# Kernel tuning notes

Hardware: AMD Instinct MI355X
Metric: run time of the kernel (lower is better)

Reference implementation:

```python
import jax, jax.numpy as jnp
import numpy as np

B, L, D, DIN, A, V, R = 1024, 100, 256, 704, 128, 32000, 129


def setup_inputs() -> dict:
    key = jax.random.key(0)
    ks = jax.random.split(key, 18)
    s = 0.05
    inp = {
        "x": jax.random.normal(ks[0], (B, DIN), jnp.float32),
        "h0": jax.random.normal(ks[1], (B, D), jnp.float32),
        "c0": jax.random.normal(ks[2], (B, D), jnp.float32),
        "src_enc": jax.random.normal(ks[3], (B, L, D), jnp.float32),
        "src_token_ids": jax.random.randint(ks[4], (B, L), 0, V),
        "W_ih": jax.random.normal(ks[5], (4 * D, DIN), jnp.float32) * s,
        "b_ih": jax.random.normal(ks[6], (4 * D,), jnp.float32) * s,
        "W_hh": jax.random.normal(ks[7], (4 * D, D), jnp.float32) * s,
        "b_hh": jax.random.normal(ks[8], (4 * D,), jnp.float32) * s,
        "W_attn": jax.random.normal(ks[9], (D, D), jnp.float32) * s,
        "W_att_vec": jax.random.normal(ks[10], (A * 2, 2 * D), jnp.float32) * s,
        "W_ptr": jax.random.normal(ks[11], (D, D), jnp.float32) * s,
        "rule_emb": jax.random.normal(ks[12], (R, 128), jnp.float32) * s,
        "W_rule_proj": jax.random.normal(ks[13], (D, 128), jnp.float32) * s,
        "prim_emb": jax.random.normal(ks[14], (V, 128), jnp.float32) * s,
        "W_prim_proj": jax.random.normal(ks[15], (D, 128), jnp.float32) * s,
        "w_gen": jax.random.normal(ks[16], (2, D), jnp.float32) * s,
        "b_gen": jax.random.normal(ks[17], (2,), jnp.float32) * s,
    }
    # W_att_vec maps concat(h, ctx) [2D] -> ATT (=256); keep shape (256, 512)
    inp["W_att_vec"] = inp["W_att_vec"][:256]
    return inp


def reference(x, h0, c0, src_enc, src_token_ids, W_ih, b_ih, W_hh, b_hh,
              W_attn, W_att_vec, W_ptr, rule_emb, W_rule_proj,
              prim_emb, W_prim_proj, w_gen, b_gen):
    # --- LSTMCell (torch gate order i, f, g, o) ---
    gates = x @ W_ih.T + b_ih + h0 @ W_hh.T + b_hh          # [B, 4D]
    i, f, g, o = jnp.split(gates, 4, axis=-1)
    i, f, o = jax.nn.sigmoid(i), jax.nn.sigmoid(f), jax.nn.sigmoid(o)
    c = f * c0 + i * jnp.tanh(g)
    h = o * jnp.tanh(c)                                      # [B, D]

    # --- dot-product attention over source encodings ---
    enc_proj = src_enc @ W_attn.T                            # [B, L, D]
    scores = jnp.einsum('bd,bld->bl', h, enc_proj)
    alpha = jax.nn.softmax(scores, axis=-1)
    ctx = jnp.einsum('bl,bld->bd', alpha, src_enc)
    att = jnp.tanh(jnp.concatenate([h, ctx], axis=-1) @ W_att_vec.T)  # [B, 256]

    # --- apply-rule (production) readout ---
    rule_proj = rule_emb @ W_rule_proj.T                     # [R, 256]
    log_p_rule = jax.nn.log_softmax(att @ rule_proj.T, axis=-1)  # [B, R]

    # --- primitive generation readout ---
    prim_proj = prim_emb @ W_prim_proj.T                     # [V, 256]
    p_gen_prim = jax.nn.softmax(att @ prim_proj.T, axis=-1)  # [B, V]

    # --- pointer network copy distribution over source positions ---
    ptr_scores = jnp.einsum('bld,bd->bl', src_enc @ W_ptr.T, att)
    copy_p = jax.nn.softmax(ptr_scores, axis=-1)             # [B, L]

    # --- gen vs copy gate (softmax over 2, per usage in parse()) ---
    gate = jax.nn.softmax(att @ w_gen.T + b_gen, axis=-1)    # [B, 2]

    # --- combined primitive distribution: gen + scattered copy mass ---
    p_prim = gate[:, :1] * p_gen_prim                        # [B, V]
    copy_mass = gate[:, 1:] * copy_p                         # [B, L]
    bidx = jnp.arange(p_prim.shape[0])[:, None]
    p_prim = p_prim.at[bidx, src_token_ids].add(copy_mass)
    return log_p_rule, p_prim, h, c, att
```

## Files before the change

### kernel.cpp

```cpp
#include <hip/hip_runtime.h>
#include <hip/hip_bf16.h>
#include <math.h>

#define NB   1024
#define LL   100
#define DD   256
#define DINN 704
#define VV   32000
#define RR   129
#define KAV  512
#define ROWU 129

typedef float f32x4 __attribute__((ext_vector_type(4)));
typedef float f32x2 __attribute__((ext_vector_type(2)));
typedef short s16x8 __attribute__((ext_vector_type(8)));
typedef unsigned short u16;
typedef unsigned int u32;

__device__ __forceinline__ float sigf(float x) { return 1.0f / (1.0f + __expf(-x)); }

__device__ __forceinline__ u16 f2bf(float f) {
    u32 u = __float_as_uint(f);
    u += 0x7fffu + ((u >> 16) & 1u);
    return (u16)(u >> 16);
}
__device__ __forceinline__ float bf2f(u16 s) {
    return __uint_as_float(((u32)s) << 16);
}

__global__ __launch_bounds__(256) void k_conv(
    const float* __restrict__ prim_emb, u16* __restrict__ prim_bf,
    const float* __restrict__ W_ih, u16* __restrict__ wih_bf,
    const float* __restrict__ W_hh, u16* __restrict__ whh_bf,
    const float* __restrict__ x, u16* __restrict__ x_bf,
    const float* __restrict__ h0, u16* __restrict__ h0_bf,
    const float* __restrict__ rule_emb, const float* __restrict__ W_rule_proj,
    float* __restrict__ rpT)
{
    __shared__ float re_s[128];
    const int bx = blockIdx.x, t = threadIdx.x;

    const float* src; u16* dst; int off;
    if (bx < 2000)      { src = prim_emb; dst = prim_bf; off = bx * 2048; }
    else if (bx < 2352) { src = W_ih;  dst = wih_bf; off = (bx - 2000) * 2048; }
    else if (bx < 2480) { src = W_hh;  dst = whh_bf; off = (bx - 2352) * 2048; }
    else if (bx < 2832) { src = x;     dst = x_bf;   off = (bx - 2480) * 2048; }
    else                { src = h0;    dst = h0_bf;  off = (bx - 2832) * 2048; }

    if (bx < RR && t < 128) re_s[t] = rule_emb[bx * 128 + t];

    int i = off + t * 8;
    f32x4 a = *reinterpret_cast<const f32x4*>(&src[i]);
    f32x4 b = *reinterpret_cast<const f32x4*>(&src[i + 4]);
    s16x8 r;
    r[0] = (short)f2bf(a[0]); r[1] = (short)f2bf(a[1]);
    r[2] = (short)f2bf(a[2]); r[3] = (short)f2bf(a[3]);
    r[4] = (short)f2bf(b[0]); r[5] = (short)f2bf(b[1]);
    r[6] = (short)f2bf(b[2]); r[7] = (short)f2bf(b[3]);
    *reinterpret_cast<s16x8*>(&dst[i]) = r;

    if (bx < RR) {
        __syncthreads();
        float acc = 0.f;
        const float* __restrict__ wr = &W_rule_proj[t * 128];
#pragma unroll 8
        for (int k = 0; k < 128; k += 4) {
            f32x4 w4 = *reinterpret_cast<const f32x4*>(&wr[k]);
            acc += w4[0] * re_s[k] + w4[1] * re_s[k + 1]
                 + w4[2] * re_s[k + 2] + w4[3] * re_s[k + 3];
        }
        rpT[t * 192 + bx] = acc;
    }
}

__global__ __launch_bounds__(256) void k_lstm(
    const u16* __restrict__ x_bf, const u16* __restrict__ h0_bf,
    const float* __restrict__ c0,
    const u16* __restrict__ wih_bf, const u16* __restrict__ whh_bf,
    const float* __restrict__ b_ih, const float* __restrict__ b_hh,
    float* __restrict__ out_h, float* __restrict__ out_c)
{
    const int t = threadIdx.x;
    const int lane = t & 63, w = t >> 6;
    const int lm = lane & 15, lq = lane >> 4;
    const int dg = blockIdx.x;
    const int row0 = blockIdx.y * 128 + w * 32;
    f32x4 acc[4][2] = {};

    for (int kt = 0; kt < 22; ++kt) {
        const int ko = kt * 32 + lq * 8;
        s16x8 bfr[4], afr[2];
#pragma unroll
        for (int mg = 0; mg < 4; ++mg)
            bfr[mg] = *reinterpret_cast<const s16x8*>(
                &wih_bf[(mg * 256 + dg * 16 + lm) * DINN + ko]);
#pragma unroll
        for (int ng = 0; ng < 2; ++ng)
            afr[ng] = *reinterpret_cast<const s16x8*>(
                &x_bf[(row0 + ng * 16 + lm) * DINN + ko]);
#pragma unroll
        for (int mg = 0; mg < 4; ++mg)
#pragma unroll
            for (int ng = 0; ng < 2; ++ng)
                acc[mg][ng] = __builtin_amdgcn_mfma_f32_16x16x32_bf16(
                    bfr[mg], afr[ng], acc[mg][ng], 0, 0, 0);
    }
    for (int kt = 0; kt < 8; ++kt) {
        const int ko = kt * 32 + lq * 8;
        s16x8 bfr[4], afr[2];
#pragma unroll
        for (int mg = 0; mg < 4; ++mg)
            bfr[mg] = *reinterpret_cast<const s16x8*>(
                &whh_bf[(mg * 256 + dg * 16 + lm) * DD + ko]);
#pragma unroll
        for (int ng = 0; ng < 2; ++ng)
            afr[ng] = *reinterpret_cast<const s16x8*>(
                &h0_bf[(row0 + ng * 16 + lm) * DD + ko]);
#pragma unroll
        for (int mg = 0; mg < 4; ++mg)
#pragma unroll
            for (int ng = 0; ng < 2; ++ng)
                acc[mg][ng] = __builtin_amdgcn_mfma_f32_16x16x32_bf16(
                    bfr[mg], afr[ng], acc[mg][ng], 0, 0, 0);
    }

    const int dc = dg * 16 + lq * 4;
    f32x4 bi[4];
#pragma unroll
    for (int mg = 0; mg < 4; ++mg) {
        f32x4 a4 = *reinterpret_cast<const f32x4*>(&b_ih[mg * 256 + dc]);
        f32x4 b4 = *reinterpret_cast<const f32x4*>(&b_hh[mg * 256 + dc]);
        bi[mg][0] = a4[0] + b4[0]; bi[mg][1] = a4[1] + b4[1];
        bi[mg][2] = a4[2] + b4[2]; bi[mg][3] = a4[3] + b4[3];
    }
#pragma unroll
    for (int ng = 0; ng < 2; ++ng) {
        const int row = row0 + ng * 16 + lm;
        f32x4 c4 = *reinterpret_cast<const f32x4*>(&c0[row * DD + dc]);
        f32x4 h4, cc4;
#pragma unroll
        for (int r = 0; r < 4; ++r) {
            float iv = acc[0][ng][r] + bi[0][r];
            float fv = acc[1][ng][r] + bi[1][r];
            float gv = acc[2][ng][r] + bi[2][r];
            float ov = acc[3][ng][r] + bi[3][r];
            float cc = sigf(fv) * c4[r] + sigf(iv) * tanhf(gv);
            cc4[r] = cc;
            h4[r] = sigf(ov) * tanhf(cc);
        }
        *reinterpret_cast<f32x4*>(&out_c[row * DD + dc]) = cc4;
        *reinterpret_cast<f32x4*>(&out_h[row * DD + dc]) = h4;
    }
}

__global__ __launch_bounds__(256) void k_hw(
    const float* __restrict__ h, const float* __restrict__ W_attn, float* __restrict__ hW)
{
    __shared__ __align__(16) float As[16][36];
    __shared__ __align__(16) float Bs[16][68];
    const int t = threadIdx.x;
    const int row0 = blockIdx.x * 32;
    const int col0 = blockIdx.y * 64;
    const int tr = t >> 4, tc = t & 15;
    float acc[2][4] = {};
    for (int kt = 0; kt < 16; ++kt) {
        __syncthreads();
#pragma unroll
        for (int p = 0; p < 2; ++p) {
            int e = t + p * 256;
            int r = e >> 4, kk = e & 15;
            As[kk][r] = h[(row0 + r) * DD + kt * 16 + kk];
        }
#pragma unroll
        for (int p = 0; p < 4; ++p) {
            int e = t + p * 256;
            int kk = e >> 6, c = e & 63;
            Bs[kk][c] = W_attn[(kt * 16 + kk) * DD + col0 + c];
        }
        __syncthreads();
#pragma unroll
        for (int kk = 0; kk < 16; ++kk) {
            float a0 = As[kk][tr * 2], a1 = As[kk][tr * 2 + 1];
            f32x4 b = *reinterpret_cast<const f32x4*>(&Bs[kk][tc * 4]);
#pragma unroll
            for (int i = 0; i < 4; ++i) {
                acc[0][i] = fmaf(a0, b[i], acc[0][i]);
                acc[1][i] = fmaf(a1, b[i], acc[1][i]);
            }
        }
    }
#pragma unroll
    for (int j = 0; j < 2; ++j) {
        f32x4 v;
#pragma unroll
        for (int i = 0; i < 4; ++i) v[i] = acc[j][i];
        *reinterpret_cast<f32x4*>(&hW[(row0 + tr * 2 + j) * DD + col0 + tc * 4]) = v;
    }
}

__global__ __launch_bounds__(256, 2) void k_attn2(
    const float* __restrict__ src_enc, const float* __restrict__ hW,
    float* __restrict__ ctx_out)
{
    __shared__ u32 enc_u[LL * ROWU];
    __shared__ __align__(16) float part[4][DD];
    __shared__ __align__(16) float hw_s[DD];
    __shared__ float sc_s[LL];
    __shared__ float al_s[LL];

    const int b = blockIdx.x, t = threadIdx.x;
    const int lane = t & 63, w = t >> 6;
    const float* __restrict__ enc = src_enc + (size_t)b * LL * DD;

    hw_s[t] = hW[b * DD + t];

#pragma unroll
    for (int p = 0; p < 25; ++p) {
        int q = p * 256 + t;
        int l = q >> 6, dq = q & 63;
        f32x4 ev = *reinterpret_cast<const f32x4*>(&enc[l * DD + dq * 4]);
        u32 w0 = (u32)f2bf(ev[0]) | ((u32)f2bf(ev[1]) << 16);
        u32 w1 = (u32)f2bf(ev[2]) | ((u32)f2bf(ev[3]) << 16);
        enc_u[l * ROWU + dq * 2]     = w0;
        enc_u[l * ROWU + dq * 2 + 1] = w1;
    }
    __syncthreads();

    {
        const int sl = ((w >> 1) << 6) + lane;
        float sp = 0.f;
        if (sl < LL) {
            const u32* __restrict__ rp = enc_u + sl * ROWU + ((w & 1) << 6);
            const float* __restrict__ hp = hw_s + ((w & 1) << 7);
#pragma unroll 32
            for (int k = 0; k < 64; ++k) {
                u32 v = rp[k];
                sp = fmaf(bf2f((u16)v),         hp[2 * k],     sp);
                sp = fmaf(bf2f((u16)(v >> 16)), hp[2 * k + 1], sp);
            }
        }
        part[w][lane] = sp;
    }
    __syncthreads();
    if (t < LL) sc_s[t] = part[(t >> 6) << 1][t & 63] + part[((t >> 6) << 1) + 1][t & 63];
    __syncthreads();

    if (w == 0) {
        float v0 = sc_s[lane];
        float v1 = (lane + 64 < LL) ? sc_s[lane + 64] : -1e30f;
        float m = fmaxf(v0, v1);
#pragma unroll
        for (int s = 1; s < 64; s <<= 1) m = fmaxf(m, __shfl_xor(m, s));
        float e0 = __expf(v0 - m);
        float e1 = (lane + 64 < LL) ? __expf(v1 - m) : 0.f;
        float ssum = e0 + e1;
#pragma unroll
        for (int s = 1; s < 64; s <<= 1) ssum += __shfl_xor(ssum, s);
        float inv = 1.f / ssum;
        al_s[lane] = e0 * inv;
        if (lane + 64 < LL) al_s[lane + 64] = e1 * inv;
    }
    __syncthreads();

    {
        const int l0 = w * 25;
        float c0 = 0.f, c1 = 0.f, c2 = 0.f, c3 = 0.f;
#pragma unroll
        for (int li = 0; li < 25; ++li) {
            int l = l0 + li;
            float a = al_s[l];
            u32 v0 = enc_u[l * ROWU + lane * 2];
            u32 v1 = enc_u[l * ROWU + lane * 2 + 1];
            c0 = fmaf(a, bf2f((u16)v0), c0);
            c1 = fmaf(a, bf2f((u16)(v0 >> 16)), c1);
            c2 = fmaf(a, bf2f((u16)v1), c2);
            c3 = fmaf(a, bf2f((u16)(v1 >> 16)), c3);
        }
        f32x4 p; p[0] = c0; p[1] = c1; p[2] = c2; p[3] = c3;
        *reinterpret_cast<f32x4*>(&part[w][lane * 4]) = p;
    }
    __syncthreads();
    ctx_out[b * DD + t] = (part[0][t] + part[1][t]) + (part[2][t] + part[3][t]);
}

__global__ __launch_bounds__(256) void k_att(
    const float* __restrict__ h, const float* __restrict__ ctx,
    const float* __restrict__ W_att_vec, float* __restrict__ att_out)
{
    __shared__ __align__(16) float As[16][36];
    __shared__ __align__(16) float Bs[16][68];
    const int t = threadIdx.x;
    const int row0 = blockIdx.x * 32;
    const int col0 = blockIdx.y * 64;
    const int tr = t >> 4, tc = t & 15;
    float acc[2][4] = {};
    for (int kt = 0; kt < 32; ++kt) {
        const float* __restrict__ Asrc = (kt < 16) ? h : ctx;
        int kb = (kt < 16) ? kt * 16 : (kt - 16) * 16;
        int kg = kt * 16;
        __syncthreads();
#pragma unroll
        for (int p = 0; p < 2; ++p) {
            int e = t + p * 256;
            int r = e >> 4, kk = e & 15;
            As[kk][r] = Asrc[(row0 + r) * DD + kb + kk];
        }
#pragma unroll
        for (int p = 0; p < 4; ++p) {
            int e = t + p * 256;
            int r = e >> 4, kk = e & 15;
            Bs[kk][r] = W_att_vec[(col0 + r) * KAV + kg + kk];
        }
        __syncthreads();
#pragma unroll
        for (int kk = 0; kk < 16; ++kk) {
            float a0 = As[kk][tr * 2], a1 = As[kk][tr * 2 + 1];
            f32x4 b = *reinterpret_cast<const f32x4*>(&Bs[kk][tc * 4]);
#pragma unroll
            for (int i = 0; i < 4; ++i) {
                acc[0][i] = fmaf(a0, b[i], acc[0][i]);
                acc[1][i] = fmaf(a1, b[i], acc[1][i]);
            }
        }
    }
#pragma unroll
    for (int j = 0; j < 2; ++j)
#pragma unroll
        for (int i = 0; i < 4; ++i)
            att_out[(row0 + tr * 2 + j) * DD + col0 + tc * 4 + i] = tanhf(acc[j][i]);
}

__global__ __launch_bounds__(256) void k_ptrproj(
    const float* __restrict__ att, const float* __restrict__ W_ptr,
    const float* __restrict__ W_prim_proj, const float* __restrict__ rpT,
    float* __restrict__ atw, u16* __restrict__ att_bf, float* __restrict__ rl)
{
    __shared__ __align__(16) float As[16][36];
    __shared__ __align__(16) float Bs[16][68];
    const int t = threadIdx.x;
    const int row0 = blockIdx.x * 32;
    const int col0 = blockIdx.y * 64;
    const int tr = t >> 4, tc = t & 15;
    float acc[2][4] = {};
    for (int kt = 0; kt < 16; ++kt) {
        __syncthreads();
#pragma unroll
        for (int p = 0; p < 2; ++p) {
            int e = t + p * 256;
            int r = e >> 4, kk = e & 15;
            As[kk][r] = att[(row0 + r) * DD + kt * 16 + kk];
        }
#pragma unroll
        for (int p = 0; p < 4; ++p) {
            int e = t + p * 256;
            int kk = e >> 6, c = e & 63;
            float bv;
            if (col0 < 256)      bv = W_ptr[(kt * 16 + kk) * DD + col0 + c];
            else if (col0 < 384) bv = W_prim_proj[(kt * 16 + kk) * 128 + (col0 - 256) + c];
            else {
                int rc = col0 - 384 + c;
                bv = (rc < RR) ? rpT[(kt * 16 + kk) * 192 + rc] : 0.f;
            }
            Bs[kk][c] = bv;
        }
        __syncthreads();
#pragma unroll
        for (int kk = 0; kk < 16; ++kk) {
            float a0 = As[kk][tr * 2], a1 = As[kk][tr * 2 + 1];
            f32x4 b = *reinterpret_cast<const f32x4*>(&Bs[kk][tc * 4]);
#pragma unroll
            for (int i = 0; i < 4; ++i) {
                acc[0][i] = fmaf(a0, b[i], acc[0][i]);
                acc[1][i] = fmaf(a1, b[i], acc[1][i]);
            }
        }
    }
    if (col0 < 256) {
#pragma unroll
        for (int j = 0; j < 2; ++j) {
            f32x4 v;
#pragma unroll
            for (int i = 0; i < 4; ++i) v[i] = acc[j][i];
            *reinterpret_cast<f32x4*>(&atw[(row0 + tr * 2 + j) * DD + col0 + tc * 4]) = v;
        }
    } else if (col0 < 384) {
#pragma unroll
        for (int j = 0; j < 2; ++j)
#pragma unroll
            for (int i = 0; i < 4; ++i)
                att_bf[(row0 + tr * 2 + j) * 128 + (col0 - 256) + tc * 4 + i] = f2bf(acc[j][i]);
    } else {
#pragma unroll
        for (int j = 0; j < 2; ++j)
#pragma unroll
            for (int i = 0; i < 4; ++i) {
                int rc = col0 - 384 + tc * 4 + i;
                if (rc < RR) rl[(row0 + tr * 2 + j) * 132 + rc] = acc[j][i];
            }
    }
}

__global__ __launch_bounds__(256) void k_fin(
    const float* __restrict__ rl, const float* __restrict__ att,
    const float* __restrict__ w_gen, const float* __restrict__ b_gen,
    float* __restrict__ log_p_rule, float* __restrict__ gate0_ws,
    float* __restrict__ gate1_ws)
{
    const int w = threadIdx.x >> 6, lane = threadIdx.x & 63;
    const int b = blockIdx.x * 4 + w;

    float v0 = rl[b * 132 + lane];
    float v1 = rl[b * 132 + 64 + lane];
    float v2 = (lane == 0) ? rl[b * 132 + 128] : -1e30f;
    float m = fmaxf(fmaxf(v0, v1), v2);
#pragma unroll
    for (int s = 1; s < 64; s <<= 1) m = fmaxf(m, __shfl_xor(m, s));
    float ssum = __expf(v0 - m) + __expf(v1 - m) + ((lane == 0) ? __expf(v2 - m) : 0.f);
#pragma unroll
    for (int s = 1; s < 64; s <<= 1) ssum += __shfl_xor(ssum, s);
    float ls = m + logf(ssum);
    log_p_rule[b * RR + lane] = v0 - ls;
    log_p_rule[b * RR + 64 + lane] = v1 - ls;
    if (lane == 0) log_p_rule[b * RR + 128] = v2 - ls;

    f32x4 a4 = *reinterpret_cast<const f32x4*>(&att[b * DD + lane * 4]);
    f32x4 g0 = *reinterpret_cast<const f32x4*>(&w_gen[lane * 4]);
    f32x4 g1 = *reinterpret_cast<const f32x4*>(&w_gen[DD + lane * 4]);
    float p0 = a4[0] * g0[0] + a4[1] * g0[1] + a4[2] * g0[2] + a4[3] * g0[3];
    float p1 = a4[0] * g1[0] + a4[1] * g1[1] + a4[2] * g1[2] + a4[3] * g1[3];
#pragma unroll
    for (int s = 1; s < 64; s <<= 1) { p0 += __shfl_xor(p0, s); p1 += __shfl_xor(p1, s); }
    if (lane == 0) {
        float ga = p0 + b_gen[0], gb = p1 + b_gen[1];
        float gm = fmaxf(ga, gb);
        float ea = __expf(ga - gm), eb = __expf(gb - gm);
        gate0_ws[b] = ea / (ea + eb);
        gate1_ws[b] = eb / (ea + eb);
    }
}

__global__ __launch_bounds__(256) void k_ptr2(
    const float* __restrict__ src_enc, const float* __restrict__ atw,
    const float* __restrict__ gate1_ws, float* __restrict__ copy_mass)
{
    __shared__ float sc_s[LL];
    const int b = blockIdx.x, t = threadIdx.x;
    const int lane = t & 63, w = t >> 6;
    const float* __restrict__ enc = src_enc + (size_t)b * LL * DD;
    f32x4 aw4 = *reinterpret_cast<const f32x4*>(&atw[b * DD + lane * 4]);

    for (int l = w; l < LL; l += 4) {
        f32x4 ev = *reinterpret_cast<const f32x4*>(&enc[l * DD + lane * 4]);
        float pr = aw4[0] * ev[0] + aw4[1] * ev[1] + aw4[2] * ev[2] + aw4[3] * ev[3];
#pragma unroll
        for (int m = 1; m < 64; m <<= 1) pr += __shfl_xor(pr, m);
        if (lane == 0) sc_s[l] = pr;
    }
    __syncthreads();
    if (w == 0) {
        float gate1 = gate1_ws[b];
        float v0 = sc_s[lane];
        float v1 = (lane + 64 < LL) ? sc_s[lane + 64] : -1e30f;
        float m = fmaxf(v0, v1);
#pragma unroll
        for (int s = 1; s < 64; s <<= 1) m = fmaxf(m, __shfl_xor(m, s));
        float ee0 = __expf(v0 - m);
        float ee1 = (lane + 64 < LL) ? __expf(v1 - m) : 0.f;
        float ssum = ee0 + ee1;
#pragma unroll
        for (int s = 1; s < 64; s <<= 1) ssum += __shfl_xor(ssum, s);
        float inv = 1.f / ssum;
        copy_mass[b * LL + lane] = gate1 * ee0 * inv;
        if (lane + 64 < LL) copy_mass[b * LL + lane + 64] = gate1 * ee1 * inv;
    }
}

template <int PASS>
__global__ __launch_bounds__(256) void k_prim(
    const u16* __restrict__ att_bf, const u16* __restrict__ prim_bf,
    const float* __restrict__ coef, float* __restrict__ stats, float* __restrict__ p_prim)
{
    const int t = threadIdx.x;
    const int lane = t & 63, w = t >> 6;
    const int lm = lane & 15, lq = lane >> 4;
    const int colbase = blockIdx.x * 128 + (w & 1) * 64;
    const int chunk = colbase >> 6;
    const int rowblk = blockIdx.y * 256;

    s16x8 pfr[4][4];
#pragma unroll
    for (int kg = 0; kg < 4; ++kg)
#pragma unroll
        for (int mg = 0; mg < 4; ++mg)
            pfr[kg][mg] = *reinterpret_cast<const s16x8*>(
                &prim_bf[(size_t)(colbase + mg * 16 + lm) * 128 + kg * 32 + lq * 8]);

    for (int it = 0; it < 2; ++it) {
        const int rowbase = rowblk + it * 128 + (w >> 1) * 64;
        f32x4 acc[4][4] = {};
#pragma unroll
        for (int kg = 0; kg < 4; ++kg) {
            s16x8 afr[4];
#pragma unroll
            for (int ng = 0; ng < 4; ++ng)
                afr[ng] = *reinterpret_cast<const s16x8*>(
                    &att_bf[(rowbase + ng * 16 + lm) * 128 + kg * 32 + lq * 8]);
#pragma unroll
            for (int mg = 0; mg < 4; ++mg)
#pragma unroll
                for (int ng = 0; ng < 4; ++ng)
                    acc[mg][ng] = __builtin_amdgcn_mfma_f32_16x16x32_bf16(
                        pfr[kg][mg], afr[ng], acc[mg][ng], 0, 0, 0);
        }
        if (PASS == 0) {
#pragma unroll
            for (int ng = 0; ng < 4; ++ng) {
                float se = 0.f;
#pragma unroll
                for (int mg = 0; mg < 4; ++mg)
                    se += __expf(acc[mg][ng][0]) + __expf(acc[mg][ng][1])
                        + __expf(acc[mg][ng][2]) + __expf(acc[mg][ng][3]);
                se += __shfl_xor(se, 16);
                se += __shfl_xor(se, 32);
                if (lq == 0)
                    stats[chunk * NB + rowbase + ng * 16 + lm] = se;
            }
        } else {
#pragma unroll
            for (int ng = 0; ng < 4; ++ng) {
                const int arow = rowbase + ng * 16 + lm;
                const float cf = coef[arow];
                float* __restrict__ dst = &p_prim[(size_t)arow * VV + colbase + lq * 4];
#pragma unroll
                for (int mg = 0; mg < 4; ++mg) {
                    f32x4 v;
                    v[0] = cf * __expf(acc[mg][ng][0]);
                    v[1] = cf * __expf(acc[mg][ng][1]);
                    v[2] = cf * __expf(acc[mg][ng][2]);
                    v[3] = cf * __expf(acc[mg][ng][3]);
                    *reinterpret_cast<f32x4*>(&dst[mg * 16]) = v;
                }
            }
        }
    }
}

__global__ __launch_bounds__(256) void k_combine(
    const float* __restrict__ stats, const float* __restrict__ gate0_ws,
    float* __restrict__ coef)
{
    const int row = blockIdx.x * 256 + threadIdx.x;
    float s0 = 0.f, s1 = 0.f, s2 = 0.f, s3 = 0.f;
    for (int c = 0; c < 500; c += 4) {
        s0 += stats[(c)     * NB + row];
        s1 += stats[(c + 1) * NB + row];
        s2 += stats[(c + 2) * NB + row];
        s3 += stats[(c + 3) * NB + row];
    }
    coef[row] = gate0_ws[row] / ((s0 + s1) + (s2 + s3));
}

__global__ __launch_bounds__(256) void k_scatter(
    const int* __restrict__ tok, const float* __restrict__ copy_mass, float* __restrict__ p_prim)
{
    int i = blockIdx.x * 256 + threadIdx.x;
    if (i >= NB * LL) return;
    int b = i / LL;
    atomicAdd(&p_prim[(size_t)b * VV + tok[i]], copy_mass[i]);
}

extern "C" void kernel_launch(void* const* d_in, const int* in_sizes, int n_in,
                              void* d_out, int out_size, void* d_ws, size_t ws_size,
                              hipStream_t stream)
{
    const float* x         = (const float*)d_in[0];
    const float* h0        = (const float*)d_in[1];
    const float* c0        = (const float*)d_in[2];
    const float* src_enc   = (const float*)d_in[3];
    const int*   tok       = (const int*)  d_in[4];
    const float* W_ih      = (const float*)d_in[5];
    const float* b_ih      = (const float*)d_in[6];
    const float* W_hh      = (const float*)d_in[7];
    const float* b_hh      = (const float*)d_in[8];
    const float* W_attn    = (const float*)d_in[9];
    const float* W_att_vec = (const float*)d_in[10];
    const float* W_ptr     = (const float*)d_in[11];
    const float* rule_emb  = (const float*)d_in[12];
    const float* W_rule_pr = (const float*)d_in[13];
    const float* prim_emb  = (const float*)d_in[14];
    const float* W_prim_pr = (const float*)d_in[15];
    const float* w_gen     = (const float*)d_in[16];
    const float* b_gen     = (const float*)d_in[17];

    float* out    = (float*)d_out;
    float* o_logp = out;
    float* o_pp   = out + 1024 * 129;
    float* o_h    = o_pp + (size_t)1024 * 32000;
    float* o_c    = o_h + 1024 * 256;
    float* o_att  = o_c + 1024 * 256;

    float* wsf      = (float*)d_ws;
    float* ws_rpT   = wsf;
    float* ws_rl    = ws_rpT   + 49152;
    float* ws_gate0 = ws_rl    + 135168;
    float* ws_gate1 = ws_gate0 + 1024;
    float* ws_cm    = ws_gate1 + 1024;
    float* ws_coef  = ws_cm    + 102400;
    float* ws_hw    = ws_coef  + 1024;
    float* ws_ctx   = ws_hw    + 262144;
    float* ws_atw   = ws_ctx   + 262144;
    float* ws_stats = ws_atw   + 262144;
    u16*   ub       = (u16*)(ws_stats + 512000);
    u16*   ws_attbf = ub;
    u16*   ws_primbf= ws_attbf + 131072;
    u16*   ws_xb    = ws_primbf + 4096000;
    u16*   ws_h0b   = ws_xb    + 720896;
    u16*   ws_wihb  = ws_h0b   + 262144;
    u16*   ws_whhb  = ws_wihb  + 720896;

    k_conv<<<dim3(2960), 256, 0, stream>>>(prim_emb, ws_primbf, W_ih, ws_wihb,
                                           W_hh, ws_whhb, x, ws_xb, h0, ws_h0b,
                                           rule_emb, W_rule_pr, ws_rpT);
    k_lstm<<<dim3(16, 8), 256, 0, stream>>>(ws_xb, ws_h0b, c0, ws_wihb, ws_whhb,
                                            b_ih, b_hh, o_h, o_c);
    k_hw<<<dim3(32, 4), 256, 0, stream>>>(o_h, W_attn, ws_hw);
    k_attn2<<<dim3(1024), 256, 0, stream>>>(src_enc, ws_hw, ws_ctx);
    k_att<<<dim3(32, 4), 256, 0, stream>>>(o_h, ws_ctx, W_att_vec, o_att);
    k_ptrproj<<<dim3(32, 9), 256, 0, stream>>>(o_att, W_ptr, W_prim_pr, ws_rpT,
                                               ws_atw, ws_attbf, ws_rl);
    k_fin<<<dim3(256), 256, 0, stream>>>(ws_rl, o_att, w_gen, b_gen,
                                         o_logp, ws_gate0, ws_gate1);
    k_ptr2<<<dim3(1024), 256, 0, stream>>>(src_enc, ws_atw, ws_gate1, ws_cm);
    k_prim<0><<<dim3(250, 4), 256, 0, stream>>>(ws_attbf, ws_primbf, nullptr, ws_stats, nullptr);
    k_combine<<<dim3(4), 256, 0, stream>>>(ws_stats, ws_gate0, ws_coef);
    k_prim<1><<<dim3(250, 4), 256, 0, stream>>>(ws_attbf, ws_primbf, ws_coef, nullptr, o_pp);
    k_scatter<<<dim3(400), 256, 0, stream>>>(tok, ws_cm, o_pp);
}
```

Measured before the change: 235.0 us.

## Move attention and projection GEMMs to bf16 MFMA with pre-transposed bf16 weights

```diff
diff --git a/kernel.cpp b/kernel.cpp
--- a/kernel.cpp
+++ b/kernel.cpp
@@ -12,7 +12,6 @@
 #define ROWU 129
 
 typedef float f32x4 __attribute__((ext_vector_type(4)));
-typedef float f32x2 __attribute__((ext_vector_type(2)));
 typedef short s16x8 __attribute__((ext_vector_type(8)));
 typedef unsigned short u16;
 typedef unsigned int u32;
@@ -34,18 +33,43 @@
     const float* __restrict__ W_hh, u16* __restrict__ whh_bf,
     const float* __restrict__ x, u16* __restrict__ x_bf,
     const float* __restrict__ h0, u16* __restrict__ h0_bf,
+    const float* __restrict__ W_att_vec, u16* __restrict__ wav_bf,
+    const float* __restrict__ W_attn, u16* __restrict__ wattnT,
+    const float* __restrict__ W_ptr, u16* __restrict__ wptrT,
+    const float* __restrict__ W_prim_proj, u16* __restrict__ wppT,
     const float* __restrict__ rule_emb, const float* __restrict__ W_rule_proj,
-    float* __restrict__ rpT)
+    u16* __restrict__ rp_bf)
 {
     __shared__ float re_s[128];
+    __shared__ __align__(16) float tile[64][65];
     const int bx = blockIdx.x, t = threadIdx.x;
 
+    if (bx >= 3024) {
+        const float* src; u16* dst; int S, D2, r0, c0;
+        if (bx < 3040) { int id = bx - 3024; src = W_attn; dst = wattnT;
+                         S = 256; D2 = 256; r0 = (id >> 2) * 64; c0 = (id & 3) * 64; }
+        else if (bx < 3056) { int id = bx - 3040; src = W_ptr; dst = wptrT;
+                         S = 256; D2 = 256; r0 = (id >> 2) * 64; c0 = (id & 3) * 64; }
+        else { int id = bx - 3056; src = W_prim_proj; dst = wppT;
+                         S = 128; D2 = 256; r0 = (id >> 1) * 64; c0 = (id & 1) * 64; }
+        const int rr = t >> 6, cc = t & 63;
+#pragma unroll
+        for (int p = 0; p < 16; ++p)
+            tile[rr + p * 4][cc] = src[(r0 + rr + p * 4) * S + c0 + cc];
+        __syncthreads();
+#pragma unroll
+        for (int p = 0; p < 16; ++p)
+            dst[(c0 + rr + p * 4) * D2 + r0 + cc] = f2bf(tile[cc][rr + p * 4]);
+        return;
+    }
+
     const float* src; u16* dst; int off;
-    if (bx < 2000)      { src = prim_emb; dst = prim_bf; off = bx * 2048; }
-    else if (bx < 2352) { src = W_ih;  dst = wih_bf; off = (bx - 2000) * 2048; }
-    else if (bx < 2480) { src = W_hh;  dst = whh_bf; off = (bx - 2352) * 2048; }
-    else if (bx < 2832) { src = x;     dst = x_bf;   off = (bx - 2480) * 2048; }
-    else                { src = h0;    dst = h0_bf;  off = (bx - 2832) * 2048; }
+    if (bx < 2000)      { src = prim_emb;  dst = prim_bf; off = bx * 2048; }
+    else if (bx < 2352) { src = W_ih;      dst = wih_bf;  off = (bx - 2000) * 2048; }
+    else if (bx < 2480) { src = W_hh;      dst = whh_bf;  off = (bx - 2352) * 2048; }
+    else if (bx < 2832) { src = x;         dst = x_bf;    off = (bx - 2480) * 2048; }
+    else if (bx < 2960) { src = h0;        dst = h0_bf;   off = (bx - 2832) * 2048; }
+    else                { src = W_att_vec; dst = wav_bf;  off = (bx - 2960) * 2048; }
 
     if (bx < RR && t < 128) re_s[t] = rule_emb[bx * 128 + t];
 
@@ -69,7 +93,7 @@
             acc += w4[0] * re_s[k] + w4[1] * re_s[k + 1]
                  + w4[2] * re_s[k + 2] + w4[3] * re_s[k + 3];
         }
-        rpT[t * 192 + bx] = acc;
+        rp_bf[bx * 256 + t] = f2bf(acc);
     }
 }
 
@@ -78,7 +102,8 @@
     const float* __restrict__ c0,
     const u16* __restrict__ wih_bf, const u16* __restrict__ whh_bf,
     const float* __restrict__ b_ih, const float* __restrict__ b_hh,
-    float* __restrict__ out_h, float* __restrict__ out_c)
+    float* __restrict__ out_h, float* __restrict__ out_c,
+    u16* __restrict__ h_bf)
 {
     const int t = threadIdx.x;
     const int lane = t & 63, w = t >> 6;
@@ -150,57 +175,55 @@
         }
         *reinterpret_cast<f32x4*>(&out_c[row * DD + dc]) = cc4;
         *reinterpret_cast<f32x4*>(&out_h[row * DD + dc]) = h4;
+        u32 w0 = (u32)f2bf(h4[0]) | ((u32)f2bf(h4[1]) << 16);
+        u32 w1 = (u32)f2bf(h4[2]) | ((u32)f2bf(h4[3]) << 16);
+        u32* hb = reinterpret_cast<u32*>(&h_bf[row * DD + dc]);
+        hb[0] = w0; hb[1] = w1;
     }
 }
 
 __global__ __launch_bounds__(256) void k_hw(
-    const float* __restrict__ h, const float* __restrict__ W_attn, float* __restrict__ hW)
-{
-    __shared__ __align__(16) float As[16][36];
-    __shared__ __align__(16) float Bs[16][68];
+    const u16* __restrict__ h_bf, const u16* __restrict__ wattnT,
+    float* __restrict__ hW)
+{
     const int t = threadIdx.x;
-    const int row0 = blockIdx.x * 32;
-    const int col0 = blockIdx.y * 64;
-    const int tr = t >> 4, tc = t & 15;
-    float acc[2][4] = {};
-    for (int kt = 0; kt < 16; ++kt) {
-        __syncthreads();
-#pragma unroll
-        for (int p = 0; p < 2; ++p) {
-            int e = t + p * 256;
-            int r = e >> 4, kk = e & 15;
-            As[kk][r] = h[(row0 + r) * DD + kt * 16 + kk];
-        }
-#pragma unroll
-        for (int p = 0; p < 4; ++p) {
-            int e = t + p * 256;
-            int kk = e >> 6, c = e & 63;
-            Bs[kk][c] = W_attn[(kt * 16 + kk) * DD + col0 + c];
-        }
-        __syncthreads();
-#pragma unroll
-        for (int kk = 0; kk < 16; ++kk) {
-            float a0 = As[kk][tr * 2], a1 = As[kk][tr * 2 + 1];
-            f32x4 b = *reinterpret_cast<const f32x4*>(&Bs[kk][tc * 4]);
-#pragma unroll
-            for (int i = 0; i < 4; ++i) {
-                acc[0][i] = fmaf(a0, b[i], acc[0][i]);
-                acc[1][i] = fmaf(a1, b[i], acc[1][i]);
-            }
-        }
-    }
-#pragma unroll
-    for (int j = 0; j < 2; ++j) {
-        f32x4 v;
-#pragma unroll
-        for (int i = 0; i < 4; ++i) v[i] = acc[j][i];
-        *reinterpret_cast<f32x4*>(&hW[(row0 + tr * 2 + j) * DD + col0 + tc * 4]) = v;
+    const int lane = t & 63, w = t >> 6;
+    const int lm = lane & 15, lq = lane >> 4;
+    const int colbase = blockIdx.x * 128 + (w & 1) * 64;
+    const int rowbase = blockIdx.y * 128 + (w >> 1) * 64;
+
+    f32x4 acc[4][4] = {};
+#pragma unroll
+    for (int kg = 0; kg < 8; ++kg) {
+        s16x8 pfr[4], afr[4];
+#pragma unroll
+        for (int mg = 0; mg < 4; ++mg)
+            pfr[mg] = *reinterpret_cast<const s16x8*>(
+                &wattnT[(colbase + mg * 16 + lm) * 256 + kg * 32 + lq * 8]);
+#pragma unroll
+        for (int ng = 0; ng < 4; ++ng)
+            afr[ng] = *reinterpret_cast<const s16x8*>(
+                &h_bf[(rowbase + ng * 16 + lm) * 256 + kg * 32 + lq * 8]);
+#pragma unroll
+        for (int mg = 0; mg < 4; ++mg)
+#pragma unroll
+            for (int ng = 0; ng < 4; ++ng)
+                acc[mg][ng] = __builtin_amdgcn_mfma_f32_16x16x32_bf16(
+                    pfr[mg], afr[ng], acc[mg][ng], 0, 0, 0);
+    }
+#pragma unroll
+    for (int ng = 0; ng < 4; ++ng) {
+        const int arow = rowbase + ng * 16 + lm;
+#pragma unroll
+        for (int mg = 0; mg < 4; ++mg)
+            *reinterpret_cast<f32x4*>(&hW[arow * DD + colbase + mg * 16 + lq * 4])
+                = acc[mg][ng];
     }
 }
 
 __global__ __launch_bounds__(256, 2) void k_attn2(
     const float* __restrict__ src_enc, const float* __restrict__ hW,
-    float* __restrict__ ctx_out)
+    u16* __restrict__ ctx_bf)
 {
     __shared__ u32 enc_u[LL * ROWU];
     __shared__ __align__(16) float part[4][DD];
@@ -280,123 +303,123 @@
         *reinterpret_cast<f32x4*>(&part[w][lane * 4]) = p;
     }
     __syncthreads();
-    ctx_out[b * DD + t] = (part[0][t] + part[1][t]) + (part[2][t] + part[3][t]);
+    ctx_bf[b * DD + t] = f2bf((part[0][t] + part[1][t]) + (part[2][t] + part[3][t]));
 }
 
 __global__ __launch_bounds__(256) void k_att(
-    const float* __restrict__ h, const float* __restrict__ ctx,
-    const float* __restrict__ W_att_vec, float* __restrict__ att_out)
-{
-    __shared__ __align__(16) float As[16][36];
-    __shared__ __align__(16) float Bs[16][68];
+    const u16* __restrict__ h_bf, const u16* __restrict__ ctx_bf,
+    const u16* __restrict__ wav_bf,
+    float* __restrict__ att_out, u16* __restrict__ att2_bf)
+{
     const int t = threadIdx.x;
-    const int row0 = blockIdx.x * 32;
-    const int col0 = blockIdx.y * 64;
-    const int tr = t >> 4, tc = t & 15;
-    float acc[2][4] = {};
-    for (int kt = 0; kt < 32; ++kt) {
-        const float* __restrict__ Asrc = (kt < 16) ? h : ctx;
-        int kb = (kt < 16) ? kt * 16 : (kt - 16) * 16;
-        int kg = kt * 16;
-        __syncthreads();
-#pragma unroll
-        for (int p = 0; p < 2; ++p) {
-            int e = t + p * 256;
-            int r = e >> 4, kk = e & 15;
-            As[kk][r] = Asrc[(row0 + r) * DD + kb + kk];
-        }
-#pragma unroll
-        for (int p = 0; p < 4; ++p) {
-            int e = t + p * 256;
-            int r = e >> 4, kk = e & 15;
-            Bs[kk][r] = W_att_vec[(col0 + r) * KAV + kg + kk];
-        }
-        __syncthreads();
-#pragma unroll
-        for (int kk = 0; kk < 16; ++kk) {
-            float a0 = As[kk][tr * 2], a1 = As[kk][tr * 2 + 1];
-            f32x4 b = *reinterpret_cast<const f32x4*>(&Bs[kk][tc * 4]);
-#pragma unroll
-            for (int i = 0; i < 4; ++i) {
-                acc[0][i] = fmaf(a0, b[i], acc[0][i]);
-                acc[1][i] = fmaf(a1, b[i], acc[1][i]);
+    const int lane = t & 63, w = t >> 6;
+    const int lm = lane & 15, lq = lane >> 4;
+    const int colbase = blockIdx.x * 128 + (w & 1) * 64;
+    const int rowbase = blockIdx.y * 128 + (w >> 1) * 64;
+
+    f32x4 acc[4][4] = {};
+#pragma unroll
+    for (int kg = 0; kg < 16; ++kg) {
+        const u16* __restrict__ asrc = (kg < 8) ? h_bf : ctx_bf;
+        const int ko = (kg & 7) * 32 + lq * 8;
+        s16x8 pfr[4], afr[4];
+#pragma unroll
+        for (int mg = 0; mg < 4; ++mg)
+            pfr[mg] = *reinterpret_cast<const s16x8*>(
+                &wav_bf[(colbase + mg * 16 + lm) * KAV + kg * 32 + lq * 8]);
+#pragma unroll
+        for (int ng = 0; ng < 4; ++ng)
+            afr[ng] = *reinterpret_cast<const s16x8*>(
+                &asrc[(rowbase + ng * 16 + lm) * 256 + ko]);
+#pragma unroll
+        for (int mg = 0; mg < 4; ++mg)
+#pragma unroll
+            for (int ng = 0; ng < 4; ++ng)
+                acc[mg][ng] = __builtin_amdgcn_mfma_f32_16x16x32_bf16(
+                    pfr[mg], afr[ng], acc[mg][ng], 0, 0, 0);
+    }
+#pragma unroll
+    for (int ng = 0; ng < 4; ++ng) {
+        const int arow = rowbase + ng * 16 + lm;
+#pragma unroll
+        for (int mg = 0; mg < 4; ++mg) {
+            const int col = colbase + mg * 16 + lq * 4;
+            f32x4 v;
+#pragma unroll
+            for (int r = 0; r < 4; ++r) v[r] = tanhf(acc[mg][ng][r]);
+            *reinterpret_cast<f32x4*>(&att_out[arow * DD + col]) = v;
+            u32 w0 = (u32)f2bf(v[0]) | ((u32)f2bf(v[1]) << 16);
+            u32 w1 = (u32)f2bf(v[2]) | ((u32)f2bf(v[3]) << 16);
+            u32* ab = reinterpret_cast<u32*>(&att2_bf[arow * DD + col]);
+            ab[0] = w0; ab[1] = w1;
+        }
+    }
+}
+
+__global__ __launch_bounds__(256) void k_ptrproj(
+    const u16* __restrict__ att2_bf, const u16* __restrict__ wptrT,
+    const u16* __restrict__ wppT, const u16* __restrict__ rp_bf,
+    float* __restrict__ atw, u16* __restrict__ att_bf, float* __restrict__ rl)
+{
+    const int t = threadIdx.x;
+    const int lane = t & 63, w = t >> 6;
+    const int lm = lane & 15, lq = lane >> 4;
+    const int gx = blockIdx.x;
+    const int colbase = gx * 128 + (w & 1) * 64;
+    const int rowbase = blockIdx.y * 128 + (w >> 1) * 64;
+
+    const u16* __restrict__ B;
+    int noff;
+    if (gx < 2)      { B = wptrT; noff = colbase; }
+    else if (gx < 3) { B = wppT;  noff = colbase - 256; }
+    else             { B = rp_bf; noff = colbase - 384; }
+
+    f32x4 acc[4][4] = {};
+#pragma unroll
+    for (int kg = 0; kg < 8; ++kg) {
+        s16x8 pfr[4], afr[4];
+#pragma unroll
+        for (int mg = 0; mg < 4; ++mg)
+            pfr[mg] = *reinterpret_cast<const s16x8*>(
+                &B[(noff + mg * 16 + lm) * 256 + kg * 32 + lq * 8]);
+#pragma unroll
+        for (int ng = 0; ng < 4; ++ng)
+            afr[ng] = *reinterpret_cast<const s16x8*>(
+                &att2_bf[(rowbase + ng * 16 + lm) * 256 + kg * 32 + lq * 8]);
+#pragma unroll
+        for (int mg = 0; mg < 4; ++mg)
+#pragma unroll
+            for (int ng = 0; ng < 4; ++ng)
+                acc[mg][ng] = __builtin_amdgcn_mfma_f32_16x16x32_bf16(
+                    pfr[mg], afr[ng], acc[mg][ng], 0, 0, 0);
+    }
+
+#pragma unroll
+    for (int ng = 0; ng < 4; ++ng) {
+        const int arow = rowbase + ng * 16 + lm;
+        if (gx < 2) {
+#pragma unroll
+            for (int mg = 0; mg < 4; ++mg)
+                *reinterpret_cast<f32x4*>(&atw[arow * DD + colbase + mg * 16 + lq * 4])
+                    = acc[mg][ng];
+        } else if (gx < 3) {
+#pragma unroll
+            for (int mg = 0; mg < 4; ++mg) {
+                const int col = noff + mg * 16 + lq * 4;
+                u32 w0 = (u32)f2bf(acc[mg][ng][0]) | ((u32)f2bf(acc[mg][ng][1]) << 16);
+                u32 w1 = (u32)f2bf(acc[mg][ng][2]) | ((u32)f2bf(acc[mg][ng][3]) << 16);
+                u32* ab = reinterpret_cast<u32*>(&att_bf[arow * 128 + col]);
+                ab[0] = w0; ab[1] = w1;
             }
-        }
-    }
-#pragma unroll
-    for (int j = 0; j < 2; ++j)
-#pragma unroll
-        for (int i = 0; i < 4; ++i)
-            att_out[(row0 + tr * 2 + j) * DD + col0 + tc * 4 + i] = tanhf(acc[j][i]);
-}
-
-__global__ __launch_bounds__(256) void k_ptrproj(
-    const float* __restrict__ att, const float* __restrict__ W_ptr,
-    const float* __restrict__ W_prim_proj, const float* __restrict__ rpT,
-    float* __restrict__ atw, u16* __restrict__ att_bf, float* __restrict__ rl)
-{
-    __shared__ __align__(16) float As[16][36];
-    __shared__ __align__(16) float Bs[16][68];
-    const int t = threadIdx.x;
-    const int row0 = blockIdx.x * 32;
-    const int col0 = blockIdx.y * 64;
-    const int tr = t >> 4, tc = t & 15;
-    float acc[2][4] = {};
-    for (int kt = 0; kt < 16; ++kt) {
-        __syncthreads();
-#pragma unroll
-        for (int p = 0; p < 2; ++p) {
-            int e = t + p * 256;
-            int r = e >> 4, kk = e & 15;
-            As[kk][r] = att[(row0 + r) * DD + kt * 16 + kk];
-        }
-#pragma unroll
-        for (int p = 0; p < 4; ++p) {
-            int e = t + p * 256;
-            int kk = e >> 6, c = e & 63;
-            float bv;
-            if (col0 < 256)      bv = W_ptr[(kt * 16 + kk) * DD + col0 + c];
-            else if (col0 < 384) bv = W_prim_proj[(kt * 16 + kk) * 128 + (col0 - 256) + c];
-            else {
-                int rc = col0 - 384 + c;
-                bv = (rc < RR) ? rpT[(kt * 16 + kk) * 192 + rc] : 0.f;
-            }
-            Bs[kk][c] = bv;
-        }
-        __syncthreads();
-#pragma unroll
-        for (int kk = 0; kk < 16; ++kk) {
-            float a0 = As[kk][tr * 2], a1 = As[kk][tr * 2 + 1];
-            f32x4 b = *reinterpret_cast<const f32x4*>(&Bs[kk][tc * 4]);
-#pragma unroll
-            for (int i = 0; i < 4; ++i) {
-                acc[0][i] = fmaf(a0, b[i], acc[0][i]);
-                acc[1][i] = fmaf(a1, b[i], acc[1][i]);
-            }
-        }
-    }
-    if (col0 < 256) {
-#pragma unroll
-        for (int j = 0; j < 2; ++j) {
-            f32x4 v;
-#pragma unroll
-            for (int i = 0; i < 4; ++i) v[i] = acc[j][i];
-            *reinterpret_cast<f32x4*>(&atw[(row0 + tr * 2 + j) * DD + col0 + tc * 4]) = v;
-        }
-    } else if (col0 < 384) {
-#pragma unroll
-        for (int j = 0; j < 2; ++j)
-#pragma unroll
-            for (int i = 0; i < 4; ++i)
-                att_bf[(row0 + tr * 2 + j) * 128 + (col0 - 256) + tc * 4 + i] = f2bf(acc[j][i]);
-    } else {
-#pragma unroll
-        for (int j = 0; j < 2; ++j)
-#pragma unroll
-            for (int i = 0; i < 4; ++i) {
-                int rc = col0 - 384 + tc * 4 + i;
-                if (rc < RR) rl[(row0 + tr * 2 + j) * 132 + rc] = acc[j][i];
-            }
+        } else {
+#pragma unroll
+            for (int mg = 0; mg < 4; ++mg)
+#pragma unroll
+                for (int r = 0; r < 4; ++r) {
+                    int rc = noff + mg * 16 + lq * 4 + r;
+                    if (rc < RR) rl[arow * 132 + rc] = acc[mg][ng][r];
+                }
+        }
     }
 }
 
@@ -561,7 +584,8 @@
 }
 
 __global__ __launch_bounds__(256) void k_scatter(
-    const int* __restrict__ tok, const float* __restrict__ copy_mass, float* __restrict__ p_prim)
+    const int* __restrict__ tok, const float* __restrict__ copy_mass,
+    float* __restrict__ p_prim)
 {
     int i = blockIdx.x * 256 + threadIdx.x;
     if (i >= NB * LL) return;
@@ -600,15 +624,13 @@
     float* o_att  = o_c + 1024 * 256;
 
     float* wsf      = (float*)d_ws;
-    float* ws_rpT   = wsf;
-    float* ws_rl    = ws_rpT   + 49152;
+    float* ws_rl    = wsf;
     float* ws_gate0 = ws_rl    + 135168;
     float* ws_gate1 = ws_gate0 + 1024;
     float* ws_cm    = ws_gate1 + 1024;
     float* ws_coef  = ws_cm    + 102400;
     float* ws_hw    = ws_coef  + 1024;
-    float* ws_ctx   = ws_hw    + 262144;
-    float* ws_atw   = ws_ctx   + 262144;
+    float* ws_atw   = ws_hw    + 262144;
     float* ws_stats = ws_atw   + 262144;
     u16*   ub       = (u16*)(ws_stats + 512000);
     u16*   ws_attbf = ub;
@@ -617,17 +639,27 @@
     u16*   ws_h0b   = ws_xb    + 720896;
     u16*   ws_wihb  = ws_h0b   + 262144;
     u16*   ws_whhb  = ws_wihb  + 720896;
-
-    k_conv<<<dim3(2960), 256, 0, stream>>>(prim_emb, ws_primbf, W_ih, ws_wihb,
+    u16*   ws_hbf   = ws_whhb  + 262144;
+    u16*   ws_ctxbf = ws_hbf   + 262144;
+    u16*   ws_att2  = ws_ctxbf + 262144;
+    u16*   ws_wavb  = ws_att2  + 262144;
+    u16*   ws_wattnT= ws_wavb  + 131072;
+    u16*   ws_wptrT = ws_wattnT+ 65536;
+    u16*   ws_wppT  = ws_wptrT + 65536;
+    u16*   ws_rpb   = ws_wppT  + 32768;
+
+    k_conv<<<dim3(3064), 256, 0, stream>>>(prim_emb, ws_primbf, W_ih, ws_wihb,
                                            W_hh, ws_whhb, x, ws_xb, h0, ws_h0b,
-                                           rule_emb, W_rule_pr, ws_rpT);
+                                           W_att_vec, ws_wavb, W_attn, ws_wattnT,
+                                           W_ptr, ws_wptrT, W_prim_pr, ws_wppT,
+                                           rule_emb, W_rule_pr, ws_rpb);
     k_lstm<<<dim3(16, 8), 256, 0, stream>>>(ws_xb, ws_h0b, c0, ws_wihb, ws_whhb,
-                                            b_ih, b_hh, o_h, o_c);
-    k_hw<<<dim3(32, 4), 256, 0, stream>>>(o_h, W_attn, ws_hw);
-    k_attn2<<<dim3(1024), 256, 0, stream>>>(src_enc, ws_hw, ws_ctx);
-    k_att<<<dim3(32, 4), 256, 0, stream>>>(o_h, ws_ctx, W_att_vec, o_att);
-    k_ptrproj<<<dim3(32, 9), 256, 0, stream>>>(o_att, W_ptr, W_prim_pr, ws_rpT,
-                                               ws_atw, ws_attbf, ws_rl);
+                                            b_ih, b_hh, o_h, o_c, ws_hbf);
+    k_hw<<<dim3(2, 8), 256, 0, stream>>>(ws_hbf, ws_wattnT, ws_hw);
+    k_attn2<<<dim3(1024), 256, 0, stream>>>(src_enc, ws_hw, ws_ctxbf);
+    k_att<<<dim3(2, 8), 256, 0, stream>>>(ws_hbf, ws_ctxbf, ws_wavb, o_att, ws_att2);
+    k_ptrproj<<<dim3(5, 8), 256, 0, stream>>>(ws_att2, ws_wptrT, ws_wppT, ws_rpb,
+                                              ws_atw, ws_attbf, ws_rl);
     k_fin<<<dim3(256), 256, 0, stream>>>(ws_rl, o_att, w_gen, b_gen,
                                          o_logp, ws_gate0, ws_gate1);
     k_ptr2<<<dim3(1024), 256, 0, stream>>>(src_enc, ws_atw, ws_gate1, ws_cm);
```

Result: faster. 223.3 us (-5.0%).
